# Kernel tuning notes

Hardware: AMD Instinct MI355X
Metric: run time of the kernel (lower is better)

The kernel has to match this reference:

```python
import jax, jax.numpy as jnp
import numpy as np

HEADS = 4
DIM_HEAD = 64
SCALE = DIM_HEAD ** -0.5


def setup_inputs() -> dict:
    key = jax.random.key(0)
    k1, k2, k3 = jax.random.split(key, 3)
    C = 256
    hidden = HEADS * DIM_HEAD  # 256
    x = jax.random.normal(k1, (16, C, 64, 64), dtype=jnp.float32)
    # 1x1 conv weights collapsed to [out, in] matrices
    w_qkv = jax.random.normal(k2, (3 * hidden, C), dtype=jnp.float32) * (C ** -0.5)
    w_out = jax.random.normal(k3, (C, hidden), dtype=jnp.float32) * (hidden ** -0.5)
    b_out = jnp.zeros((C,), dtype=jnp.float32)
    return {"x": x, "w_qkv": w_qkv, "w_out": w_out, "b_out": b_out}


def reference(x, w_qkv, w_out, b_out):
    b, c, h, w = x.shape
    n = h * w
    # 1x1 conv == channel GEMM
    qkv = jnp.einsum('bchw,oc->bohw', x, w_qkv)           # [b, 3*hidden, h, w]
    qkv = qkv.reshape(b, 3, HEADS, DIM_HEAD, n)            # [b, 3, H, d, n]
    q, k, v = qkv[:, 0], qkv[:, 1], qkv[:, 2]              # each [b, H, d, n]
    q = jax.nn.softmax(q, axis=2) * SCALE                  # softmax over d
    k = jax.nn.softmax(k, axis=3)                          # softmax over n
    context = jnp.einsum('bhdn,bhen->bhde', k, v)          # [b, H, d, e]
    out = jnp.einsum('bhde,bhdn->bhen', context, q)        # [b, H, e, n]
    out = out.reshape(b, HEADS * DIM_HEAD, h, w)           # [b, hidden, h, w]
    return jnp.einsum('bchw,oc->bohw', out, w_out) + b_out[None, :, None, None]
```

## Files before the change

### kernel.cpp

```cpp
#include <hip/hip_runtime.h>

#define NPIX 4096
#define SCALE 0.125f

typedef _Float16 half8 __attribute__((ext_vector_type(8)));
typedef _Float16 half4 __attribute__((ext_vector_type(4)));
typedef float floatx4 __attribute__((ext_vector_type(4)));

__device__ __forceinline__ void async16(void* lds, const void* g) {
  __builtin_amdgcn_global_load_lds(
      (const __attribute__((address_space(1))) unsigned int*)(uintptr_t)g,
      (__attribute__((address_space(3))) unsigned int*)(unsigned)(uintptr_t)lds,
      16, 0, 0);
}

__device__ __forceinline__ void vmwait(int n) {
  if (n >= 6)      asm volatile("s_waitcnt vmcnt(6)" ::: "memory");
  else if (n >= 4) asm volatile("s_waitcnt vmcnt(4)" ::: "memory");
  else             asm volatile("s_waitcnt vmcnt(0)" ::: "memory");
}

__device__ __forceinline__ void pipe_barrier(int n) {
  __builtin_amdgcn_sched_barrier(0);
  vmwait(n);
  __builtin_amdgcn_s_barrier();
  __builtin_amdgcn_sched_barrier(0);
}

__global__ __launch_bounds__(256) void split16_kernel(const float* __restrict__ w,
                                                      _Float16* __restrict__ hi,
                                                      _Float16* __restrict__ lo, int n) {
  int i = blockIdx.x * 256 + threadIdx.x;
  if (i < n) {
    float v = w[i];
    _Float16 h = (_Float16)v;
    hi[i] = h;
    lo[i] = (_Float16)(v - (float)h);
  }
}

__global__ __launch_bounds__(256) void transpose16_kernel(const float* __restrict__ x,
                                                          _Float16* __restrict__ xt) {
  __shared__ float t[64][65];
  const int n0 = blockIdx.x * 64, c0 = blockIdx.y * 64, b = blockIdx.z;
  const float* xp = x + (long)b * 256 * NPIX;
  const int tid = threadIdx.x;
  const int r = tid >> 4, c4 = (tid & 15) * 4;
#pragma unroll
  for (int p = 0; p < 4; p++) {
    float4 v = *(const float4*)&xp[(long)(c0 + r + p * 16) * NPIX + n0 + c4];
    t[r + p * 16][c4 + 0] = v.x;
    t[r + p * 16][c4 + 1] = v.y;
    t[r + p * 16][c4 + 2] = v.z;
    t[r + p * 16][c4 + 3] = v.w;
  }
  __syncthreads();
  const int n = tid >> 2, cg = (tid & 3) * 16;
  alignas(16) _Float16 o[16];
#pragma unroll
  for (int i = 0; i < 16; i++) o[i] = (_Float16)t[cg + i][n];
  _Float16* dst = &xt[((long)b * NPIX + n0 + n) * 256 + c0 + cg];
  *(float4*)dst = *(float4*)&o[0];
  *(float4*)(dst + 8) = *(float4*)&o[8];
}

__global__ __launch_bounds__(256) void q_gemm_softmax(const _Float16* __restrict__ Ahp,
                                                      const _Float16* __restrict__ Alp,
                                                      const _Float16* __restrict__ Bt,
                                                      _Float16* __restrict__ PT) {
  union alignas(16) QU {
    _Float16 st[3][3][128 * 32];
    _Float16 pt[128][128];
  };
  __shared__ QU u;
  const int tid = threadIdx.x;
  const int n0 = blockIdx.x * 128, m0 = blockIdx.y * 128;
  const int bz = blockIdx.z;
  const _Float16* Bp = Bt + (long)bz * NPIX * 256;
  const int wv = tid >> 6, l = tid & 63;
  const int r16 = l & 15, q = l >> 4;
  const int mb = (wv >> 1) * 64, nb = (wv & 1) * 64;
  const int r1 = tid >> 2;
  const int o1 = ((tid & 3) * 8) ^ (((r1 >> 1) & 3) * 8);
  const int r2 = r1 + 64;
  const int ldsc1 = (wv * 64) * 8;
  const int ldsc2 = (256 + wv * 64) * 8;
  const int q8 = (q * 8) ^ (((r16 >> 1) & 3) * 8);

  auto STAGE = [&](int buf, int kt) {
    const int k0 = kt * 32;
    async16(&u.st[buf][0][ldsc1], &Ahp[(long)(m0 + r1) * 256 + k0 + o1]);
    async16(&u.st[buf][0][ldsc2], &Ahp[(long)(m0 + r2) * 256 + k0 + o1]);
    async16(&u.st[buf][1][ldsc1], &Alp[(long)(m0 + r1) * 256 + k0 + o1]);
    async16(&u.st[buf][1][ldsc2], &Alp[(long)(m0 + r2) * 256 + k0 + o1]);
    async16(&u.st[buf][2][ldsc1], &Bp[(long)(n0 + r1) * 256 + k0 + o1]);
    async16(&u.st[buf][2][ldsc2], &Bp[(long)(n0 + r2) * 256 + k0 + o1]);
  };

  floatx4 acc[4][4];
#pragma unroll
  for (int i = 0; i < 4; i++)
#pragma unroll
    for (int j = 0; j < 4; j++) acc[i][j] = (floatx4){0.f, 0.f, 0.f, 0.f};

  STAGE(0, 0);
  STAGE(1, 1);
  pipe_barrier(6);
  int cc = 0;
  for (int kt = 0; kt < 8; kt++) {
    if (kt < 6) {
      int sb = cc + 2;
      if (sb >= 3) sb -= 3;
      STAGE(sb, kt + 2);
    }
    half8 fa[4], flo[4], fb[4];
#pragma unroll
    for (int i = 0; i < 4; i++) {
      fa[i] = *(const half8*)&u.st[cc][0][(mb + i * 16 + r16) * 32 + q8];
      flo[i] = *(const half8*)&u.st[cc][1][(mb + i * 16 + r16) * 32 + q8];
      fb[i] = *(const half8*)&u.st[cc][2][(nb + i * 16 + r16) * 32 + q8];
    }
#pragma unroll
    for (int i = 0; i < 4; i++)
#pragma unroll
      for (int j = 0; j < 4; j++) {
        acc[i][j] = __builtin_amdgcn_mfma_f32_16x16x32_f16(fa[i], fb[j], acc[i][j], 0, 0, 0);
        acc[i][j] = __builtin_amdgcn_mfma_f32_16x16x32_f16(flo[i], fb[j], acc[i][j], 0, 0, 0);
      }
    pipe_barrier(kt < 6 ? 6 : 0);
    cc = (cc == 2) ? 0 : cc + 1;
  }

#pragma unroll
  for (int j = 0; j < 4; j++) {
    float s = 0.f;
#pragma unroll
    for (int i = 0; i < 4; i++)
#pragma unroll
      for (int t = 0; t < 4; t++) {
        float e = __expf(acc[i][j][t]);
        acc[i][j][t] = e;
        s += e;
      }
    s += __shfl_xor(s, 16, 64);
    s += __shfl_xor(s, 32, 64);
    const float rinv = 1.0f / s;
    const int nl = nb + j * 16 + r16;
    const int swz = (nl & 7) * 8;
#pragma unroll
    for (int i = 0; i < 4; i++) {
      half4 h4;
#pragma unroll
      for (int t = 0; t < 4; t++) h4[t] = (_Float16)(acc[i][j][t] * rinv);
      *(half4*)&u.pt[nl][(mb + i * 16 + q * 4) ^ swz] = h4;
    }
  }
  __syncthreads();
  const int rbase = tid >> 4, c16 = tid & 15;
  _Float16* dst = PT + ((long)(bz * 2 + (m0 >> 7)) * NPIX + n0) * 128;
#pragma unroll
  for (int k = 0; k < 8; k++) {
    const int row = rbase + k * 16;
    const int chunk = c16 ^ (row & 7);
    float4 v = *(const float4*)&u.pt[row][chunk * 8];
    *(float4*)&dst[(long)row * 128 + c16 * 8] = v;
  }
}

#define CPB 2
__global__ __launch_bounds__(256) void kv_ctx_gemm(const _Float16* __restrict__ Ahp,
                                                   const _Float16* __restrict__ Bt,
                                                   float* __restrict__ pbuf,
                                                   float* __restrict__ rsbuf) {
  union alignas(16) KVU {
    _Float16 st[3][2][128 * 32];
    _Float16 ev[128][136];
  };
  __shared__ KVU u;
  const int tid = threadIdx.x;
  const int cg = blockIdx.x;
  const int hi = blockIdx.y;
  const int b = blockIdx.z;
  const _Float16* Bp = Bt + (long)b * NPIX * 256;
  const int wv = tid >> 6, l = tid & 63;
  const int r16 = l & 15, q = l >> 4;
  const int mb = (wv >> 1) * 64, nb = (wv & 1) * 64;
  const int r1 = tid >> 2;
  const int o1 = ((tid & 3) * 8) ^ (((r1 >> 1) & 3) * 8);
  const int ldsc1 = (wv * 64) * 8;
  const int ldsc2 = (256 + wv * 64) * 8;
  const int q8 = (q * 8) ^ (((r16 >> 1) & 3) * 8);
  const long gAk = (long)(256 + hi * 64 + r1) * 256;
  const long gAv = (long)(512 + hi * 64 + r1) * 256;

  auto STAGE = [&](int buf, int kt, int n0) {
    const int k0 = kt * 32;
    async16(&u.st[buf][0][ldsc1], &Ahp[gAk + k0 + o1]);
    async16(&u.st[buf][0][ldsc2], &Ahp[gAv + k0 + o1]);
    async16(&u.st[buf][1][ldsc1], &Bp[(long)(n0 + r1) * 256 + k0 + o1]);
    async16(&u.st[buf][1][ldsc2], &Bp[(long)(n0 + 64 + r1) * 256 + k0 + o1]);
  };

  floatx4 c2[4];
#pragma unroll
  for (int j = 0; j < 4; j++) c2[j] = (floatx4){0.f, 0.f, 0.f, 0.f};
  float rs = 0.f;

  for (int cs = 0; cs < CPB; cs++) {
    const int n0 = (cg * CPB + cs) * 128;
    floatx4 acc[4][4];
#pragma unroll
    for (int i = 0; i < 4; i++)
#pragma unroll
      for (int j = 0; j < 4; j++) acc[i][j] = (floatx4){0.f, 0.f, 0.f, 0.f};

    STAGE(0, 0, n0);
    STAGE(1, 1, n0);
    pipe_barrier(4);
    int cc = 0;
    for (int kt = 0; kt < 8; kt++) {
      if (kt < 6) {
        int sb = cc + 2;
        if (sb >= 3) sb -= 3;
        STAGE(sb, kt + 2, n0);
      }
      half8 fa[4], fb[4];
#pragma unroll
      for (int i = 0; i < 4; i++) {
        fa[i] = *(const half8*)&u.st[cc][0][(mb + i * 16 + r16) * 32 + q8];
        fb[i] = *(const half8*)&u.st[cc][1][(nb + i * 16 + r16) * 32 + q8];
      }
#pragma unroll
      for (int i = 0; i < 4; i++)
#pragma unroll
        for (int j = 0; j < 4; j++)
          acc[i][j] = __builtin_amdgcn_mfma_f32_16x16x32_f16(fa[i], fb[j], acc[i][j], 0, 0, 0);
      pipe_barrier(kt < 6 ? 4 : 0);
      cc = (cc == 2) ? 0 : cc + 1;
    }

    const bool is_k = (mb == 0);
#pragma unroll
    for (int i = 0; i < 4; i++) {
      const int row = mb + i * 16 + q * 4;
#pragma unroll
      for (int j = 0; j < 4; j++) {
        const int col = nb + j * 16 + r16;
#pragma unroll
        for (int t = 0; t < 4; t++) {
          const float vv0 = acc[i][j][t];
          u.ev[row + t][col] = (_Float16)(is_k ? __expf(vv0) : vv0);
        }
      }
    }
    __syncthreads();

#pragma unroll
    for (int ks = 0; ks < 4; ks++) {
      half8 a = *(const half8*)&u.ev[wv * 16 + r16][ks * 32 + q * 8];
#pragma unroll
      for (int ii = 0; ii < 8; ii++) rs += (float)a[ii];
#pragma unroll
      for (int j = 0; j < 4; j++) {
        half8 bv = *(const half8*)&u.ev[64 + j * 16 + r16][ks * 32 + q * 8];
        c2[j] = __builtin_amdgcn_mfma_f32_16x16x32_f16(a, bv, c2[j], 0, 0, 0);
      }
    }
    __syncthreads();
  }

  rs += __shfl_xor(rs, 16, 64);
  rs += __shfl_xor(rs, 32, 64);
  const int bh = b * 4 + hi;
  float* pp = pbuf + ((long)bh * 16 + cg) * 4096;
#pragma unroll
  for (int j = 0; j < 4; j++)
#pragma unroll
    for (int reg = 0; reg < 4; reg++)
      pp[(wv * 16 + q * 4 + reg) * 64 + j * 16 + r16] = c2[j][reg];
  if (l < 16) rsbuf[((long)bh * 16 + cg) * 64 + wv * 16 + r16] = rs;
}

__global__ __launch_bounds__(256) void mctx_fused(const float* __restrict__ w_out,
                                                  const float* __restrict__ pbuf,
                                                  const float* __restrict__ rsbuf,
                                                  _Float16* __restrict__ Mhi,
                                                  _Float16* __restrict__ Mlo) {
  __shared__ float sctxT[64][65];
  __shared__ float sinv[64];
  const int cq = blockIdx.x, h = blockIdx.y, b = blockIdx.z;
  const int bh = b * 4 + h;
  const float* pp = pbuf + (long)bh * 16 * 4096;
  const int tid = threadIdx.x;
  {
    const int d = tid >> 2, e0 = (tid & 3) * 16;
    float s0[16];
#pragma unroll
    for (int i = 0; i < 16; i++) s0[i] = 0.f;
    for (int c = 0; c < 16; c++) {
#pragma unroll
      for (int k = 0; k < 4; k++) {
        float4 v = *(const float4*)&pp[(long)c * 4096 + d * 64 + e0 + k * 4];
        s0[k * 4 + 0] += v.x;
        s0[k * 4 + 1] += v.y;
        s0[k * 4 + 2] += v.z;
        s0[k * 4 + 3] += v.w;
      }
    }
#pragma unroll
    for (int i = 0; i < 16; i++) sctxT[e0 + i][d] = s0[i];
  }
  if (tid < 64) {
    const float* rp = rsbuf + (long)bh * 16 * 64 + tid;
    float z = 0.f;
#pragma unroll
    for (int c = 0; c < 16; c++) z += rp[c * 64];
    sinv[tid] = 1.0f / z;
  }
  __syncthreads();
  const int c = cq * 64 + (tid >> 2);
  const int d0 = (tid & 3) * 16;
  const float* wp = w_out + (long)c * 256 + h * 64;
  float acc[16];
#pragma unroll
  for (int i = 0; i < 16; i++) acc[i] = 0.f;
#pragma unroll
  for (int e4 = 0; e4 < 16; e4++) {
    float4 wv = *(const float4*)&wp[e4 * 4];
#pragma unroll
    for (int u2 = 0; u2 < 4; u2++) {
      const float we = ((const float*)&wv)[u2];
      const int e = e4 * 4 + u2;
#pragma unroll
      for (int dd = 0; dd < 16; dd++) acc[dd] = fmaf(we, sctxT[e][d0 + dd], acc[dd]);
    }
  }
  alignas(16) _Float16 hi16[16], lo16[16];
#pragma unroll
  for (int k4 = 0; k4 < 4; k4++) {
    float4 zv = *(const float4*)&sinv[d0 + k4 * 4];
#pragma unroll
    for (int u2 = 0; u2 < 4; u2++) {
      const int dd = k4 * 4 + u2;
      float v = acc[dd] * (SCALE * ((const float*)&zv)[u2]);
      _Float16 hh = (_Float16)v;
      hi16[dd] = hh;
      lo16[dd] = (_Float16)(v - (float)hh);
    }
  }
  _Float16* mh = Mhi + ((long)b * 256 + c) * 256 + h * 64 + d0;
  _Float16* ml = Mlo + ((long)b * 256 + c) * 256 + h * 64 + d0;
#pragma unroll
  for (int k = 0; k < 2; k++) {
    *(float4*)&mh[k * 8] = *(float4*)&hi16[k * 8];
    *(float4*)&ml[k * 8] = *(float4*)&lo16[k * 8];
  }
}

__global__ __launch_bounds__(256) void out_gemm(const _Float16* __restrict__ Mhi,
                                                const _Float16* __restrict__ Mlo,
                                                const _Float16* __restrict__ PT,
                                                float* __restrict__ C,
                                                const float* __restrict__ bias) {
  __shared__ _Float16 st[3][3][128 * 32];
  const int tid = threadIdx.x;
  const int n0 = blockIdx.x * 128, m0 = blockIdx.y * 128;
  const int b = blockIdx.z;
  const _Float16* Ah = Mhi + (long)b * 65536;
  const _Float16* Al = Mlo + (long)b * 65536;
  float* Cp = C + (long)b * 256 * NPIX;
  const int wv = tid >> 6, l = tid & 63;
  const int r16 = l & 15, q = l >> 4;
  const int mb = (wv >> 1) * 64, nb = (wv & 1) * 64;
  const int r1 = tid >> 2;
  const int o1 = ((tid & 3) * 8) ^ (((r1 >> 1) & 3) * 8);
  const int r2 = r1 + 64;
  const int ldsc1 = (wv * 64) * 8;
  const int ldsc2 = (256 + wv * 64) * 8;
  const int q8 = (q * 8) ^ (((r16 >> 1) & 3) * 8);

  auto STAGE = [&](int buf, int kt) {
    const int k0 = kt * 32;
    async16(&st[buf][0][ldsc1], &Ah[(long)(m0 + r1) * 256 + k0 + o1]);
    async16(&st[buf][0][ldsc2], &Ah[(long)(m0 + r2) * 256 + k0 + o1]);
    async16(&st[buf][1][ldsc1], &Al[(long)(m0 + r1) * 256 + k0 + o1]);
    async16(&st[buf][1][ldsc2], &Al[(long)(m0 + r2) * 256 + k0 + o1]);
    const _Float16* Bk = PT + ((long)(b * 2 + (kt >> 2)) * NPIX + n0) * 128;
    async16(&st[buf][2][ldsc1], &Bk[(long)r1 * 128 + (kt & 3) * 32 + o1]);
    async16(&st[buf][2][ldsc2], &Bk[(long)(r1 + 64) * 128 + (kt & 3) * 32 + o1]);
  };

  floatx4 acc[4][4];
#pragma unroll
  for (int i = 0; i < 4; i++)
#pragma unroll
    for (int j = 0; j < 4; j++) acc[i][j] = (floatx4){0.f, 0.f, 0.f, 0.f};

  STAGE(0, 0);
  STAGE(1, 1);
  pipe_barrier(6);
  int cc = 0;
  for (int kt = 0; kt < 8; kt++) {
    if (kt < 6) {
      int sb = cc + 2;
      if (sb >= 3) sb -= 3;
      STAGE(sb, kt + 2);
    }
    half8 fa[4], flo[4], fb[4];
#pragma unroll
    for (int i = 0; i < 4; i++) {
      fa[i] = *(const half8*)&st[cc][0][(mb + i * 16 + r16) * 32 + q8];
      flo[i] = *(const half8*)&st[cc][1][(mb + i * 16 + r16) * 32 + q8];
      fb[i] = *(const half8*)&st[cc][2][(nb + i * 16 + r16) * 32 + q8];
    }
#pragma unroll
    for (int i = 0; i < 4; i++)
#pragma unroll
      for (int j = 0; j < 4; j++) {
        acc[i][j] = __builtin_amdgcn_mfma_f32_16x16x32_f16(fa[i], fb[j], acc[i][j], 0, 0, 0);
        acc[i][j] = __builtin_amdgcn_mfma_f32_16x16x32_f16(flo[i], fb[j], acc[i][j], 0, 0, 0);
      }
    pipe_barrier(kt < 6 ? 6 : 0);
    cc = (cc == 2) ? 0 : cc + 1;
  }
#pragma unroll
  for (int i = 0; i < 4; i++) {
    const int mrow = m0 + mb + i * 16 + q * 4;
#pragma unroll
    for (int t = 0; t < 4; t++) {
      float bz = bias[mrow + t];
#pragma unroll
      for (int j = 0; j < 4; j++) {
        Cp[(long)(mrow + t) * NPIX + n0 + nb + j * 16 + r16] = acc[i][j][t] + bz;
      }
    }
  }
}

extern "C" void kernel_launch(void* const* d_in, const int* in_sizes, int n_in,
                              void* d_out, int out_size, void* d_ws, size_t ws_size,
                              hipStream_t stream) {
  const float* x = (const float*)d_in[0];
  const float* w_qkv = (const float*)d_in[1];
  const float* w_out = (const float*)d_in[2];
  const float* b_out = (const float*)d_in[3];
  float* out = (float*)d_out;

  _Float16* PT = (_Float16*)d_ws;
  float* rsbuf = (float*)(PT + (long)16 * 2 * NPIX * 128);
  _Float16* wq_hi = (_Float16*)(rsbuf + 64 * 16 * 64);
  _Float16* wq_lo = wq_hi + 768 * 256;
  _Float16* Mhi = wq_lo + 768 * 256;
  _Float16* Mlo = Mhi + 16 * 256 * 256;
  _Float16* xt = (_Float16*)d_out;
  float* pbuf = (float*)d_out + (1 << 23);

  split16_kernel<<<768, 256, 0, stream>>>(w_qkv, wq_hi, wq_lo, 768 * 256);
  transpose16_kernel<<<dim3(64, 4, 16), 256, 0, stream>>>(x, xt);
  kv_ctx_gemm<<<dim3(16, 4, 16), 256, 0, stream>>>(wq_hi, xt, pbuf, rsbuf);
  mctx_fused<<<dim3(4, 4, 16), 256, 0, stream>>>(w_out, pbuf, rsbuf, Mhi, Mlo);
  q_gemm_softmax<<<dim3(32, 2, 16), 256, 0, stream>>>(wq_hi, wq_lo, xt, PT);
  out_gemm<<<dim3(32, 2, 16), 256, 0, stream>>>(Mhi, Mlo, PT, out, b_out);
}
```

Baseline: 209.6 us.

## Fuse q projection softmax and output GEMM into one kernel

Merges the Q-GEMM+softmax kernel and the output GEMM into a single 512-thread block per 128-pixel tile. The softmaxed P tile stays in LDS instead of round-tripping through global memory. This removes the PT write/read and one kernel launch. In exchange the blocks are larger, use more LDS, and switch from a 3-stage async pipeline to double buffering with full __syncthreads. The xt and pbuf buffers move from the output buffer to the workspace, since the output is now written by the same kernel that reads xt.

```diff
diff --git a/kernel.cpp b/kernel.cpp
--- a/kernel.cpp
+++ b/kernel.cpp
@@ -62,109 +62,6 @@
   _Float16* dst = &xt[((long)b * NPIX + n0 + n) * 256 + c0 + cg];
   *(float4*)dst = *(float4*)&o[0];
   *(float4*)(dst + 8) = *(float4*)&o[8];
-}
-
-__global__ __launch_bounds__(256) void q_gemm_softmax(const _Float16* __restrict__ Ahp,
-                                                      const _Float16* __restrict__ Alp,
-                                                      const _Float16* __restrict__ Bt,
-                                                      _Float16* __restrict__ PT) {
-  union alignas(16) QU {
-    _Float16 st[3][3][128 * 32];
-    _Float16 pt[128][128];
-  };
-  __shared__ QU u;
-  const int tid = threadIdx.x;
-  const int n0 = blockIdx.x * 128, m0 = blockIdx.y * 128;
-  const int bz = blockIdx.z;
-  const _Float16* Bp = Bt + (long)bz * NPIX * 256;
-  const int wv = tid >> 6, l = tid & 63;
-  const int r16 = l & 15, q = l >> 4;
-  const int mb = (wv >> 1) * 64, nb = (wv & 1) * 64;
-  const int r1 = tid >> 2;
-  const int o1 = ((tid & 3) * 8) ^ (((r1 >> 1) & 3) * 8);
-  const int r2 = r1 + 64;
-  const int ldsc1 = (wv * 64) * 8;
-  const int ldsc2 = (256 + wv * 64) * 8;
-  const int q8 = (q * 8) ^ (((r16 >> 1) & 3) * 8);
-
-  auto STAGE = [&](int buf, int kt) {
-    const int k0 = kt * 32;
-    async16(&u.st[buf][0][ldsc1], &Ahp[(long)(m0 + r1) * 256 + k0 + o1]);
-    async16(&u.st[buf][0][ldsc2], &Ahp[(long)(m0 + r2) * 256 + k0 + o1]);
-    async16(&u.st[buf][1][ldsc1], &Alp[(long)(m0 + r1) * 256 + k0 + o1]);
-    async16(&u.st[buf][1][ldsc2], &Alp[(long)(m0 + r2) * 256 + k0 + o1]);
-    async16(&u.st[buf][2][ldsc1], &Bp[(long)(n0 + r1) * 256 + k0 + o1]);
-    async16(&u.st[buf][2][ldsc2], &Bp[(long)(n0 + r2) * 256 + k0 + o1]);
-  };
-
-  floatx4 acc[4][4];
-#pragma unroll
-  for (int i = 0; i < 4; i++)
-#pragma unroll
-    for (int j = 0; j < 4; j++) acc[i][j] = (floatx4){0.f, 0.f, 0.f, 0.f};
-
-  STAGE(0, 0);
-  STAGE(1, 1);
-  pipe_barrier(6);
-  int cc = 0;
-  for (int kt = 0; kt < 8; kt++) {
-    if (kt < 6) {
-      int sb = cc + 2;
-      if (sb >= 3) sb -= 3;
-      STAGE(sb, kt + 2);
-    }
-    half8 fa[4], flo[4], fb[4];
-#pragma unroll
-    for (int i = 0; i < 4; i++) {
-      fa[i] = *(const half8*)&u.st[cc][0][(mb + i * 16 + r16) * 32 + q8];
-      flo[i] = *(const half8*)&u.st[cc][1][(mb + i * 16 + r16) * 32 + q8];
-      fb[i] = *(const half8*)&u.st[cc][2][(nb + i * 16 + r16) * 32 + q8];
-    }
-#pragma unroll
-    for (int i = 0; i < 4; i++)
-#pragma unroll
-      for (int j = 0; j < 4; j++) {
-        acc[i][j] = __builtin_amdgcn_mfma_f32_16x16x32_f16(fa[i], fb[j], acc[i][j], 0, 0, 0);
-        acc[i][j] = __builtin_amdgcn_mfma_f32_16x16x32_f16(flo[i], fb[j], acc[i][j], 0, 0, 0);
-      }
-    pipe_barrier(kt < 6 ? 6 : 0);
-    cc = (cc == 2) ? 0 : cc + 1;
-  }
-
-#pragma unroll
-  for (int j = 0; j < 4; j++) {
-    float s = 0.f;
-#pragma unroll
-    for (int i = 0; i < 4; i++)
-#pragma unroll
-      for (int t = 0; t < 4; t++) {
-        float e = __expf(acc[i][j][t]);
-        acc[i][j][t] = e;
-        s += e;
-      }
-    s += __shfl_xor(s, 16, 64);
-    s += __shfl_xor(s, 32, 64);
-    const float rinv = 1.0f / s;
-    const int nl = nb + j * 16 + r16;
-    const int swz = (nl & 7) * 8;
-#pragma unroll
-    for (int i = 0; i < 4; i++) {
-      half4 h4;
-#pragma unroll
-      for (int t = 0; t < 4; t++) h4[t] = (_Float16)(acc[i][j][t] * rinv);
-      *(half4*)&u.pt[nl][(mb + i * 16 + q * 4) ^ swz] = h4;
-    }
-  }
-  __syncthreads();
-  const int rbase = tid >> 4, c16 = tid & 15;
-  _Float16* dst = PT + ((long)(bz * 2 + (m0 >> 7)) * NPIX + n0) * 128;
-#pragma unroll
-  for (int k = 0; k < 8; k++) {
-    const int row = rbase + k * 16;
-    const int chunk = c16 ^ (row & 7);
-    float4 v = *(const float4*)&u.pt[row][chunk * 8];
-    *(float4*)&dst[(long)row * 128 + c16 * 8] = v;
-  }
 }
 
 #define CPB 2
@@ -357,38 +254,49 @@
   }
 }
 
-__global__ __launch_bounds__(256) void out_gemm(const _Float16* __restrict__ Mhi,
-                                                const _Float16* __restrict__ Mlo,
-                                                const _Float16* __restrict__ PT,
-                                                float* __restrict__ C,
-                                                const float* __restrict__ bias) {
-  __shared__ _Float16 st[3][3][128 * 32];
+__global__ __launch_bounds__(512) void qout_fused(const _Float16* __restrict__ wqh,
+                                                  const _Float16* __restrict__ wql,
+                                                  const _Float16* __restrict__ xt,
+                                                  const _Float16* __restrict__ Mhi,
+                                                  const _Float16* __restrict__ Mlo,
+                                                  const float* __restrict__ bias,
+                                                  float* __restrict__ out) {
+  struct alignas(16) QO {
+    _Float16 st[2][20480];
+    _Float16 P[128][256];
+  };
+  __shared__ QO u;
   const int tid = threadIdx.x;
-  const int n0 = blockIdx.x * 128, m0 = blockIdx.y * 128;
-  const int b = blockIdx.z;
-  const _Float16* Ah = Mhi + (long)b * 65536;
-  const _Float16* Al = Mlo + (long)b * 65536;
-  float* Cp = C + (long)b * 256 * NPIX;
+  const int n0 = blockIdx.x * 128;
+  const int b = blockIdx.y;
+  const _Float16* Bp = xt + (long)b * NPIX * 256;
+  const _Float16* MhB = Mhi + (long)b * 65536;
+  const _Float16* MlB = Mlo + (long)b * 65536;
+  float* Cp = out + (long)b * 256 * NPIX;
   const int wv = tid >> 6, l = tid & 63;
   const int r16 = l & 15, q = l >> 4;
-  const int mb = (wv >> 1) * 64, nb = (wv & 1) * 64;
+  const int mb = (wv >> 1) * 64;
+  const int nb = (wv & 1) * 64;
   const int r1 = tid >> 2;
   const int o1 = ((tid & 3) * 8) ^ (((r1 >> 1) & 3) * 8);
-  const int r2 = r1 + 64;
-  const int ldsc1 = (wv * 64) * 8;
-  const int ldsc2 = (256 + wv * 64) * 8;
+  const int ldsW = wv * 512;
   const int q8 = (q * 8) ^ (((r16 >> 1) & 3) * 8);
 
-  auto STAGE = [&](int buf, int kt) {
+  auto STAGE1 = [&](int buf, int kt) {
     const int k0 = kt * 32;
-    async16(&st[buf][0][ldsc1], &Ah[(long)(m0 + r1) * 256 + k0 + o1]);
-    async16(&st[buf][0][ldsc2], &Ah[(long)(m0 + r2) * 256 + k0 + o1]);
-    async16(&st[buf][1][ldsc1], &Al[(long)(m0 + r1) * 256 + k0 + o1]);
-    async16(&st[buf][1][ldsc2], &Al[(long)(m0 + r2) * 256 + k0 + o1]);
-    const _Float16* Bk = PT + ((long)(b * 2 + (kt >> 2)) * NPIX + n0) * 128;
-    async16(&st[buf][2][ldsc1], &Bk[(long)r1 * 128 + (kt & 3) * 32 + o1]);
-    async16(&st[buf][2][ldsc2], &Bk[(long)(r1 + 64) * 128 + (kt & 3) * 32 + o1]);
+    async16(&u.st[buf][0 + ldsW], &wqh[(long)r1 * 256 + k0 + o1]);
+    async16(&u.st[buf][4096 + ldsW], &wqh[(long)(128 + r1) * 256 + k0 + o1]);
+    async16(&u.st[buf][8192 + ldsW], &wql[(long)r1 * 256 + k0 + o1]);
+    async16(&u.st[buf][12288 + ldsW], &wql[(long)(128 + r1) * 256 + k0 + o1]);
+    async16(&u.st[buf][16384 + ldsW], &Bp[(long)(n0 + r1) * 256 + k0 + o1]);
   };
+  auto STAGE2 = [&](int buf, int kt) {
+    const int k0 = kt * 32;
+    async16(&u.st[buf][0 + ldsW], &MhB[(long)r1 * 256 + k0 + o1]);
+    async16(&u.st[buf][4096 + ldsW], &MhB[(long)(128 + r1) * 256 + k0 + o1]);
+    async16(&u.st[buf][8192 + ldsW], &MlB[(long)r1 * 256 + k0 + o1]);
+    async16(&u.st[buf][12288 + ldsW], &MlB[(long)(128 + r1) * 256 + k0 + o1]);
+  };
 
   floatx4 acc[4][4];
 #pragma unroll
@@ -396,22 +304,17 @@
 #pragma unroll
     for (int j = 0; j < 4; j++) acc[i][j] = (floatx4){0.f, 0.f, 0.f, 0.f};
 
-  STAGE(0, 0);
-  STAGE(1, 1);
-  pipe_barrier(6);
-  int cc = 0;
+  STAGE1(0, 0);
+  __syncthreads();
   for (int kt = 0; kt < 8; kt++) {
-    if (kt < 6) {
-      int sb = cc + 2;
-      if (sb >= 3) sb -= 3;
-      STAGE(sb, kt + 2);
-    }
+    const int cur = kt & 1;
+    if (kt < 7) STAGE1(cur ^ 1, kt + 1);
     half8 fa[4], flo[4], fb[4];
 #pragma unroll
     for (int i = 0; i < 4; i++) {
-      fa[i] = *(const half8*)&st[cc][0][(mb + i * 16 + r16) * 32 + q8];
-      flo[i] = *(const half8*)&st[cc][1][(mb + i * 16 + r16) * 32 + q8];
-      fb[i] = *(const half8*)&st[cc][2][(nb + i * 16 + r16) * 32 + q8];
+      fa[i] = *(const half8*)&u.st[cur][(mb + i * 16 + r16) * 32 + q8];
+      flo[i] = *(const half8*)&u.st[cur][8192 + (mb + i * 16 + r16) * 32 + q8];
+      fb[i] = *(const half8*)&u.st[cur][16384 + (nb + i * 16 + r16) * 32 + q8];
     }
 #pragma unroll
     for (int i = 0; i < 4; i++)
@@ -420,18 +323,73 @@
         acc[i][j] = __builtin_amdgcn_mfma_f32_16x16x32_f16(fa[i], fb[j], acc[i][j], 0, 0, 0);
         acc[i][j] = __builtin_amdgcn_mfma_f32_16x16x32_f16(flo[i], fb[j], acc[i][j], 0, 0, 0);
       }
-    pipe_barrier(kt < 6 ? 6 : 0);
-    cc = (cc == 2) ? 0 : cc + 1;
-  }
+    __syncthreads();
+  }
+
+  STAGE2(0, 0);
+
+#pragma unroll
+  for (int j = 0; j < 4; j++) {
+    float s = 0.f;
+#pragma unroll
+    for (int i = 0; i < 4; i++)
+#pragma unroll
+      for (int t = 0; t < 4; t++) {
+        float e = __expf(acc[i][j][t]);
+        acc[i][j][t] = e;
+        s += e;
+      }
+    s += __shfl_xor(s, 16, 64);
+    s += __shfl_xor(s, 32, 64);
+    const float rinv = 1.0f / s;
+    const int nl = nb + j * 16 + r16;
+    const int swz = (nl & 7) * 8;
+#pragma unroll
+    for (int i = 0; i < 4; i++) {
+      half4 h4;
+#pragma unroll
+      for (int t = 0; t < 4; t++) h4[t] = (_Float16)(acc[i][j][t] * rinv);
+      *(half4*)&u.P[nl][(mb + i * 16 + q * 4) ^ swz] = h4;
+    }
+  }
+  __syncthreads();
+
+  floatx4 ac2[4][4];
+#pragma unroll
+  for (int i = 0; i < 4; i++)
+#pragma unroll
+    for (int j = 0; j < 4; j++) ac2[i][j] = (floatx4){0.f, 0.f, 0.f, 0.f};
+
+  for (int kt = 0; kt < 8; kt++) {
+    const int cur = kt & 1;
+    if (kt < 7) STAGE2(cur ^ 1, kt + 1);
+    half8 fa[4], flo[4], fb[4];
+#pragma unroll
+    for (int i = 0; i < 4; i++) {
+      fa[i] = *(const half8*)&u.st[cur][(mb + i * 16 + r16) * 32 + q8];
+      flo[i] = *(const half8*)&u.st[cur][8192 + (mb + i * 16 + r16) * 32 + q8];
+      const int nrow = nb + i * 16 + r16;
+      fb[i] = *(const half8*)&u.P[nrow][(kt * 32 + q * 8) ^ ((nrow & 7) * 8)];
+    }
+#pragma unroll
+    for (int i = 0; i < 4; i++)
+#pragma unroll
+      for (int j = 0; j < 4; j++) {
+        ac2[i][j] = __builtin_amdgcn_mfma_f32_16x16x32_f16(fa[i], fb[j], ac2[i][j], 0, 0, 0);
+        ac2[i][j] = __builtin_amdgcn_mfma_f32_16x16x32_f16(flo[i], fb[j], ac2[i][j], 0, 0, 0);
+      }
+    __syncthreads();
+  }
+
 #pragma unroll
   for (int i = 0; i < 4; i++) {
-    const int mrow = m0 + mb + i * 16 + q * 4;
+    const int mrow = mb + i * 16 + q * 4;
 #pragma unroll
     for (int t = 0; t < 4; t++) {
       float bz = bias[mrow + t];
 #pragma unroll
       for (int j = 0; j < 4; j++) {
-        Cp[(long)(mrow + t) * NPIX + n0 + nb + j * 16 + r16] = acc[i][j][t] + bz;
+        Cp[(long)(mrow + t) * NPIX + n0 + nb + j * 16 + r16] = ac2[i][j][t] + bz;
       }
     }
   }
@@ -446,19 +404,17 @@
   const float* b_out = (const float*)d_in[3];
   float* out = (float*)d_out;
 
-  _Float16* PT = (_Float16*)d_ws;
-  float* rsbuf = (float*)(PT + (long)16 * 2 * NPIX * 128);
+  _Float16* xt = (_Float16*)d_ws;
+  float* pbuf = (float*)(xt + (long)16 * NPIX * 256);
+  float* rsbuf = pbuf + (long)64 * 16 * 4096;
   _Float16* wq_hi = (_Float16*)(rsbuf + 64 * 16 * 64);
   _Float16* wq_lo = wq_hi + 768 * 256;
   _Float16* Mhi = wq_lo + 768 * 256;
   _Float16* Mlo = Mhi + 16 * 256 * 256;
-  _Float16* xt = (_Float16*)d_out;
-  float* pbuf = (float*)d_out + (1 << 23);
 
   split16_kernel<<<768, 256, 0, stream>>>(w_qkv, wq_hi, wq_lo, 768 * 256);
   transpose16_kernel<<<dim3(64, 4, 16), 256, 0, stream>>>(x, xt);
   kv_ctx_gemm<<<dim3(16, 4, 16), 256, 0, stream>>>(wq_hi, xt, pbuf, rsbuf);
   mctx_fused<<<dim3(4, 4, 16), 256, 0, stream>>>(w_out, pbuf, rsbuf, Mhi, Mlo);
-  q_gemm_softmax<<<dim3(32, 2, 16), 256, 0, stream>>>(wq_hi, wq_lo, xt, PT);
-  out_gemm<<<dim3(32, 2, 16), 256, 0, stream>>>(Mhi, Mlo, PT, out, b_out);
-}
+  qout_fused<<<dim3(32, 16), 512, 0, stream>>>(wq_hi, wq_lo, xt, Mhi, Mlo, b_out, out);
+}
```

Result: faster. 200.8 us (-4.2%).
